# Kernel optimization log

Hardware: AMD Instinct MI355X
Metric: run time of the kernel (lower is better)

## Reference

```python
import jax, jax.numpy as jnp
import numpy as np

N_NODES = 50000
N_EDGES = 1600000
N_GRAPHS = 64
F_IN = 256
H = 1024
EPS = 1e-5


def setup_inputs() -> dict:
    key = jax.random.key(0)
    ks = jax.random.split(key, 6)
    x = jax.random.normal(ks[0], (N_NODES, F_IN), dtype=jnp.float32)
    edge_index = jax.random.randint(ks[1], (2, N_EDGES), 0, N_NODES, dtype=jnp.int32)
    batch = jnp.sort(jax.random.randint(ks[2], (N_NODES,), 0, N_GRAPHS, dtype=jnp.int32))
    # Glorot-ish init for GCN weights
    W0 = jax.random.normal(ks[3], (F_IN, H), dtype=jnp.float32) * (1.0 / np.sqrt(F_IN))
    b0 = jnp.zeros((H,), dtype=jnp.float32)
    Ws = jax.random.normal(ks[4], (3, H, H), dtype=jnp.float32) * (1.0 / np.sqrt(H))
    bs = jnp.zeros((3, H), dtype=jnp.float32)
    gammas = jnp.ones((4, H), dtype=jnp.float32)
    betas = jnp.zeros((4, H), dtype=jnp.float32)
    return {"x": x, "edge_index": edge_index, "batch": batch,
            "W0": W0, "b0": b0, "Ws": Ws, "bs": bs,
            "gammas": gammas, "betas": betas}


def _gcn_norm(edge_index, n_nodes):
    # Add self-loops (PyG GCNConv default), compute symmetric normalization.
    loops = jnp.arange(n_nodes, dtype=edge_index.dtype)
    row = jnp.concatenate([edge_index[0], loops])  # sources
    col = jnp.concatenate([edge_index[1], loops])  # targets (aggregation index)
    ones = jnp.ones(row.shape[0], dtype=jnp.float32)
    deg = jax.ops.segment_sum(ones, col, num_segments=n_nodes)
    dinv = jnp.where(deg > 0, jax.lax.rsqrt(deg), 0.0)
    norm = dinv[row] * dinv[col]  # [E + N]
    return row, col, norm


def _layer(h, W, b, gamma, beta, row, col, norm):
    ht = h @ W                                           # [N, H] GEMM
    msg = ht[row] * norm[:, None]                        # gather + scale
    agg = jax.ops.segment_sum(msg, col, num_segments=N_NODES) + b
    mu = jnp.mean(agg, axis=-1, keepdims=True)
    var = jnp.mean(jnp.square(agg - mu), axis=-1, keepdims=True)
    hn = (agg - mu) * jax.lax.rsqrt(var + EPS) * gamma + beta
    return jax.nn.relu(hn)


def reference(x, edge_index, batch, W0, b0, Ws, bs, gammas, betas):
    row, col, norm = _gcn_norm(edge_index, N_NODES)
    h = _layer(x, W0, b0, gammas[0], betas[0], row, col, norm)
    for i in range(3):
        h = _layer(h, Ws[i], bs[i], gammas[i + 1], betas[i + 1], row, col, norm)
    # scatter_mean over batch (graph-level pooling)
    sums = jax.ops.segment_sum(h, batch, num_segments=N_GRAPHS)
    cnt = jax.ops.segment_sum(jnp.ones((N_NODES,), jnp.float32), batch, num_segments=N_GRAPHS)
    return sums / jnp.maximum(cnt, 1.0)[:, None]
```

## Files before the change

kernel.cpp:

```cpp
#include <hip/hip_runtime.h>
#include <hip/hip_bf16.h>
#include <stdint.h>

#define NN 50000
#define NE 1600000
#define NG 64
#define FIN 256
#define HD 1024
#define EPSV 1e-5f

typedef __bf16 bf16;
typedef float f32x4 __attribute__((ext_vector_type(4)));
typedef float f32x2 __attribute__((ext_vector_type(2)));
typedef int i32x4 __attribute__((ext_vector_type(4)));

typedef const __attribute__((address_space(1))) void* gptr_as1;
typedef __attribute__((address_space(3))) void* lptr_as3;

__device__ __forceinline__ void load_g2l_16(const void* g, const void* l) {
  __builtin_amdgcn_global_load_lds((gptr_as1)(uintptr_t)g,
                                   (lptr_as3)(uint32_t)(uintptr_t)l, 16, 0, 0);
}

__global__ void hist_kernel(const int* __restrict__ col, int* __restrict__ cnt, int E) {
  int e = blockIdx.x * 256 + threadIdx.x;
  if (e < E) atomicAdd(&cnt[col[e]], 1);
}

__global__ void dinv_kernel(const int* __restrict__ cnt, float* __restrict__ dinv, int n) {
  int i = blockIdx.x * 256 + threadIdx.x;
  if (i < n) dinv[i] = rsqrtf((float)(cnt[i] + 1));
}

__global__ void scan_partial_kernel(const int* __restrict__ cnt, int* __restrict__ partial, int n) {
  __shared__ int red[4];
  int i = blockIdx.x * 256 + threadIdx.x;
  int v = (i < n) ? cnt[i] : 0;
  #pragma unroll
  for (int off = 32; off; off >>= 1) v += __shfl_down(v, off, 64);
  if ((threadIdx.x & 63) == 0) red[threadIdx.x >> 6] = v;
  __syncthreads();
  if (threadIdx.x == 0) partial[blockIdx.x] = red[0] + red[1] + red[2] + red[3];
}

__global__ void scan_scan_kernel(int* __restrict__ partial, int nb) {
  __shared__ int s[256];
  int t = threadIdx.x;
  int v = (t < nb) ? partial[t] : 0;
  s[t] = v;
  __syncthreads();
  for (int off = 1; off < 256; off <<= 1) {
    int x = (t >= off) ? s[t - off] : 0;
    __syncthreads();
    s[t] += x;
    __syncthreads();
  }
  if (t < nb) partial[t] = s[t] - v;
}

__global__ void scan_final_kernel(const int* __restrict__ cnt, const int* __restrict__ partial,
                                  int* __restrict__ row_ptr, int n, int E) {
  __shared__ int s[256];
  int t = threadIdx.x;
  int i = blockIdx.x * 256 + t;
  int v = (i < n) ? cnt[i] : 0;
  s[t] = v;
  __syncthreads();
  for (int off = 1; off < 256; off <<= 1) {
    int x = (t >= off) ? s[t - off] : 0;
    __syncthreads();
    s[t] += x;
    __syncthreads();
  }
  if (i < n) row_ptr[i] = partial[blockIdx.x] + s[t] - v;
  if (i == 0) row_ptr[n] = E;
}

__global__ void scatter_kernel(const int* __restrict__ rowi, const int* __restrict__ coli,
                               const int* __restrict__ row_ptr, int* __restrict__ fill,
                               const float* __restrict__ dinv,
                               int2* __restrict__ csr_sw, int E) {
  int e = blockIdx.x * 256 + threadIdx.x;
  if (e >= E) return;
  int s = rowi[e], d = coli[e];
  int pos = row_ptr[d] + atomicAdd(&fill[d], 1);
  int2 p;
  p.x = s;
  p.y = __float_as_int(dinv[s] * dinv[d]);
  csr_sw[pos] = p;
}

__global__ __launch_bounds__(256) void quant_x_kernel(const float* __restrict__ x,
                                                      int8_t* __restrict__ A8,
                                                      float* __restrict__ hscale) {
  int row = blockIdx.x * 4 + (threadIdx.x >> 6);
  int t = threadIdx.x & 63;
  float4 v = ((const float4*)(x + (size_t)row * FIN))[t];
  float m = fmaxf(fmaxf(fabsf(v.x), fabsf(v.y)), fmaxf(fabsf(v.z), fabsf(v.w)));
  #pragma unroll
  for (int off = 32; off; off >>= 1) m = fmaxf(m, __shfl_xor(m, off, 64));
  float inv = (m > 0.f) ? 127.0f / m : 0.f;
  int q0 = min(127, max(-127, __float2int_rn(v.x * inv)));
  int q1 = min(127, max(-127, __float2int_rn(v.y * inv)));
  int q2 = min(127, max(-127, __float2int_rn(v.z * inv)));
  int q3 = min(127, max(-127, __float2int_rn(v.w * inv)));
  uint32_t p = ((uint32_t)(q0 & 0xff)) | ((uint32_t)(q1 & 0xff) << 8) |
               ((uint32_t)(q2 & 0xff) << 16) | ((uint32_t)(q3 & 0xff) << 24);
  ((uint32_t*)A8)[(size_t)row * 64 + t] = p;
  if (t == 0) hscale[row] = (m > 0.f) ? m / 127.0f : 0.f;
}

__device__ __forceinline__ const float* layer_W(const float* W0, const float* Ws, int L) {
  return (L == 0) ? W0 : Ws + (size_t)(L - 1) * HD * HD;
}

__global__ void wamax_all_kernel(const float* __restrict__ W0, const float* __restrict__ Ws,
                                 uint32_t* __restrict__ colmax) {
  __shared__ float lds[8][32];
  int L = blockIdx.z;
  int K = (L == 0) ? FIN : HD;
  int k0 = blockIdx.y * 128;
  if (k0 >= K) return;
  const float* W = layer_W(W0, Ws, L);
  int n = blockIdx.x * 32 + threadIdx.x;
  int kend = min(k0 + 128, K);
  float m = 0.f;
  for (int k = k0 + threadIdx.y; k < kend; k += 8)
    m = fmaxf(m, fabsf(W[(size_t)k * HD + n]));
  lds[threadIdx.y][threadIdx.x] = m;
  __syncthreads();
  if (threadIdx.y == 0) {
    #pragma unroll
    for (int i = 1; i < 8; i++) m = fmaxf(m, lds[i][threadIdx.x]);
    atomicMax(&colmax[L * HD + n], __float_as_uint(m));
  }
}

__global__ void wscale_all_kernel(const uint32_t* __restrict__ colmax,
                                  float* __restrict__ wscale) {
  int i = blockIdx.x * 256 + threadIdx.x;
  if (i < 4 * HD) {
    float m = __uint_as_float(colmax[i]);
    wscale[i] = (m > 0.f) ? m / 127.0f : 0.f;
  }
}

__global__ void transpose_wq8_all_kernel(const float* __restrict__ W0,
                                         const float* __restrict__ Ws,
                                         const uint32_t* __restrict__ colmax,
                                         int8_t* __restrict__ Wt8_all) {
  __shared__ float tile[32][33];
  int L = blockIdx.z;
  int K = (L == 0) ? FIN : HD;
  int k0 = blockIdx.y * 32;
  if (k0 >= K) return;
  const float* W = layer_W(W0, Ws, L);
  int8_t* Wt8 = Wt8_all + ((L == 0) ? 0 : (size_t)FIN * HD + (size_t)(L - 1) * HD * HD);
  int n0 = blockIdx.x * 32;
  int tx = threadIdx.x, ty = threadIdx.y;
  #pragma unroll
  for (int i = ty; i < 32; i += 8) tile[i][tx] = W[(size_t)(k0 + i) * HD + n0 + tx];
  __syncthreads();
  #pragma unroll
  for (int i = ty; i < 32; i += 8) {
    float cm = __uint_as_float(colmax[L * HD + n0 + i]);
    float inv = (cm > 0.f) ? 127.0f / cm : 0.f;
    int q = min(127, max(-127, __float2int_rn(tile[tx][i] * inv)));
    Wt8[(size_t)(n0 + i) * K + k0 + tx] = (int8_t)q;
  }
}

__global__ __launch_bounds__(256, 4) void gemm_i8_q8_kernel(
    const int8_t* __restrict__ A8, const float* __restrict__ hscale,
    const int8_t* __restrict__ Wt8, const float* __restrict__ wscale,
    uint8_t* __restrict__ C8, float* __restrict__ scales, int M, int K) {
  __shared__ __align__(16) int8_t As[2][128 * 64];
  __shared__ __align__(16) int8_t Bs[2][128 * 64];
  __shared__ float smax[2][128];
  const int tid = threadIdx.x;
  const int w = tid >> 6, l = tid & 63;

  const int nwg = gridDim.x;
  const int o = blockIdx.x;
  const int lid = (o & 7) * (nwg >> 3) + (o >> 3);
  const int m0 = (lid >> 3) * 128, n0 = (lid & 7) * 128;
  const int cb = lid & 7;
  const int wr = w >> 1, wc = w & 1;

  i32x4 acc[4][4] = {};

  const int r0 = tid >> 2;
  const int c16 = (tid & 3) * 16;
  int ar0 = m0 + r0;       if (ar0 >= M) ar0 = M - 1;
  int ar1 = m0 + r0 + 64;  if (ar1 >= M) ar1 = M - 1;
  const int8_t* a0 = A8 + (size_t)ar0 * K + c16;
  const int8_t* a1 = A8 + (size_t)ar1 * K + c16;
  const int8_t* b0 = Wt8 + (size_t)(n0 + r0) * K + c16;
  const int8_t* b1 = Wt8 + (size_t)(n0 + r0 + 64) * K + c16;

  const int mrow = l & 15;
  const int kch = (l >> 4) * 16;

  auto stage = [&](int b, int k) {
    int8_t* asw = &As[b][w * 1024];
    int8_t* bsw = &Bs[b][w * 1024];
    load_g2l_16(a0 + k, asw);
    load_g2l_16(a1 + k, asw + 4096);
    load_g2l_16(b0 + k, bsw);
    load_g2l_16(b1 + k, bsw + 4096);
  };

  const int nit = K >> 6;
  stage(0, 0);
  __syncthreads();

  int cur = 0;
  for (int t = 0; t < nit; ++t) {
    if (t + 1 < nit) stage(cur ^ 1, (t + 1) << 6);
    i32x4 af[4], bf_[4];
    #pragma unroll
    for (int m = 0; m < 4; m++)
      af[m] = *(const i32x4*)&As[cur][(wr * 64 + m * 16 + mrow) * 64 + kch];
    #pragma unroll
    for (int n = 0; n < 4; n++)
      bf_[n] = *(const i32x4*)&Bs[cur][(wc * 64 + n * 16 + mrow) * 64 + kch];
    #pragma unroll
    for (int m = 0; m < 4; m++)
      #pragma unroll
      for (int n = 0; n < 4; n++)
        acc[m][n] = __builtin_amdgcn_mfma_i32_16x16x64_i8(af[m], bf_[n], acc[m][n], 0, 0, 0);
    __syncthreads();
    cur ^= 1;
  }

  float wsv[4];
  #pragma unroll
  for (int n = 0; n < 4; n++) wsv[n] = wscale[n0 + wc * 64 + n * 16 + (l & 15)];

  #pragma unroll
  for (int m = 0; m < 4; m++) {
    #pragma unroll
    for (int r = 0; r < 4; r++) {
      int rl = wr * 64 + m * 16 + (l >> 4) * 4 + r;
      int grow = m0 + rl; if (grow >= M) grow = M - 1;
      float v = 0.f;
      #pragma unroll
      for (int n = 0; n < 4; n++)
        v = fmaxf(v, fabsf((float)acc[m][n][r] * wsv[n]));
      v *= hscale[grow];
      #pragma unroll
      for (int mask = 1; mask < 16; mask <<= 1) v = fmaxf(v, __shfl_xor(v, mask, 64));
      if ((l & 15) == 0) smax[wc][rl] = v;
    }
  }
  __syncthreads();

  #pragma unroll
  for (int m = 0; m < 4; m++) {
    #pragma unroll
    for (int r = 0; r < 4; r++) {
      int rl = wr * 64 + m * 16 + (l >> 4) * 4 + r;
      int grow = m0 + rl;
      float mx = fmaxf(smax[0][rl], smax[1][rl]);
      float inv = (mx > 0.f) ? 127.0f / mx : 0.f;
      if (grow < M) {
        float hs = hscale[grow];
        if (wc == 0 && (l & 15) == 0)
          scales[(size_t)grow * 8 + cb] = (mx > 0.f) ? mx / 127.0f : 0.f;
        #pragma unroll
        for (int n = 0; n < 4; n++) {
          int gcol = n0 + wc * 64 + n * 16 + (l & 15);
          int u = __float2int_rn((float)acc[m][n][r] * hs * wsv[n] * inv) + 128;
          C8[(size_t)grow * HD + gcol] = (uint8_t)u;
        }
      }
    }
  }
}

__device__ __forceinline__ void acc_u8p(f32x2 a[4], float& sw, float w, uint2 d) {
  sw += w;
  f32x2 w2 = {w, w};
  f32x2 v0 = {(float)(d.x & 0xffu), (float)((d.x >> 8) & 0xffu)};
  f32x2 v1 = {(float)((d.x >> 16) & 0xffu), (float)(d.x >> 24)};
  f32x2 v2 = {(float)(d.y & 0xffu), (float)((d.y >> 8) & 0xffu)};
  f32x2 v3 = {(float)((d.y >> 16) & 0xffu), (float)(d.y >> 24)};
  a[0] += w2 * v0;
  a[1] += w2 * v1;
  a[2] += w2 * v2;
  a[3] += w2 * v3;
}

__global__ __launch_bounds__(256) void agg_ln_u8_kernel(
    const uint8_t* __restrict__ htu8, const float* __restrict__ scales,
    const int* __restrict__ row_ptr, const int2* __restrict__ csr_sw,
    const float* __restrict__ dinv, const float* __restrict__ bias,
    const float* __restrict__ gamma, const float* __restrict__ beta,
    int8_t* __restrict__ hq, float* __restrict__ hscale) {
  const int g = threadIdx.x >> 7;
  const int node = blockIdx.x * 2 + g;
  const int tt = threadIdx.x & 127;
  const int cbL = tt >> 4;
  const int wid = threadIdx.x >> 6;
  __shared__ float red[4];

  f32x2 acc2[4] = {};
  float sw = 0.f;

  float dn = dinv[node];
  float wself = dn * dn * scales[(size_t)node * 8 + cbL];
  acc_u8p(acc2, sw, wself, ((const uint2*)(htu8 + (size_t)node * HD))[tt]);

  int e = row_ptr[node];
  const int e1 = row_ptr[node + 1];
  for (; e + 4 <= e1; e += 4) {
    int2 p0 = csr_sw[e], p1 = csr_sw[e + 1], p2 = csr_sw[e + 2], p3 = csr_sw[e + 3];
    float w0 = __int_as_float(p0.y) * scales[(size_t)p0.x * 8 + cbL];
    float w1 = __int_as_float(p1.y) * scales[(size_t)p1.x * 8 + cbL];
    float w2 = __int_as_float(p2.y) * scales[(size_t)p2.x * 8 + cbL];
    float w3 = __int_as_float(p3.y) * scales[(size_t)p3.x * 8 + cbL];
    uint2 d0 = ((const uint2*)(htu8 + (size_t)p0.x * HD))[tt];
    uint2 d1 = ((const uint2*)(htu8 + (size_t)p1.x * HD))[tt];
    uint2 d2 = ((const uint2*)(htu8 + (size_t)p2.x * HD))[tt];
    uint2 d3 = ((const uint2*)(htu8 + (size_t)p3.x * HD))[tt];
    acc_u8p(acc2, sw, w0, d0);
    acc_u8p(acc2, sw, w1, d1);
    acc_u8p(acc2, sw, w2, d2);
    acc_u8p(acc2, sw, w3, d3);
  }
  for (; e < e1; e++) {
    int2 p = csr_sw[e];
    float wgt = __int_as_float(p.y) * scales[(size_t)p.x * 8 + cbL];
    acc_u8p(acc2, sw, wgt, ((const uint2*)(htu8 + (size_t)p.x * HD))[tt]);
  }

  float acc[8] = {acc2[0][0], acc2[0][1], acc2[1][0], acc2[1][1],
                  acc2[2][0], acc2[2][1], acc2[3][0], acc2[3][1]};

  const float4* bias2 = (const float4*)bias;
  float4 ba = bias2[tt * 2], bb = bias2[tt * 2 + 1];
  float c128 = 128.0f * sw;
  acc[0] += ba.x - c128; acc[1] += ba.y - c128; acc[2] += ba.z - c128; acc[3] += ba.w - c128;
  acc[4] += bb.x - c128; acc[5] += bb.y - c128; acc[6] += bb.z - c128; acc[7] += bb.w - c128;

  float s = 0.f;
  #pragma unroll
  for (int j = 0; j < 8; j++) s += acc[j];
  #pragma unroll
  for (int off = 32; off; off >>= 1) s += __shfl_down(s, off, 64);
  if ((threadIdx.x & 63) == 0) red[wid] = s;
  __syncthreads();
  float mean = (red[g * 2] + red[g * 2 + 1]) * (1.0f / HD);
  __syncthreads();

  float d[8], s2 = 0.f;
  #pragma unroll
  for (int j = 0; j < 8; j++) { d[j] = acc[j] - mean; s2 += d[j] * d[j]; }
  #pragma unroll
  for (int off = 32; off; off >>= 1) s2 += __shfl_down(s2, off, 64);
  if ((threadIdx.x & 63) == 0) red[wid] = s2;
  __syncthreads();
  float var = (red[g * 2] + red[g * 2 + 1]) * (1.0f / HD);
  float rstd = rsqrtf(var + EPSV);

  const float4* gam2 = (const float4*)gamma;
  const float4* bet2 = (const float4*)beta;
  float4 g0 = gam2[tt * 2], g1 = gam2[tt * 2 + 1];
  float4 be0 = bet2[tt * 2], be1 = bet2[tt * 2 + 1];
  float gv[8] = {g0.x, g0.y, g0.z, g0.w, g1.x, g1.y, g1.z, g1.w};
  float bv[8] = {be0.x, be0.y, be0.z, be0.w, be1.x, be1.y, be1.z, be1.w};
  float o[8];
  float rmax = 0.f;
  #pragma unroll
  for (int j = 0; j < 8; j++) {
    o[j] = fmaxf(d[j] * rstd * gv[j] + bv[j], 0.0f);
    rmax = fmaxf(rmax, o[j]);
  }

  __syncthreads();
  #pragma unroll
  for (int off = 32; off; off >>= 1) rmax = fmaxf(rmax, __shfl_xor(rmax, off, 64));
  if ((threadIdx.x & 63) == 0) red[wid] = rmax;
  __syncthreads();
  float rm = fmaxf(red[g * 2], red[g * 2 + 1]);
  float qinv = (rm > 0.f) ? 127.0f / rm : 0.f;
  int q[8];
  #pragma unroll
  for (int j = 0; j < 8; j++) q[j] = min(127, __float2int_rn(o[j] * qinv));
  uint32_t p0 = ((uint32_t)q[0]) | ((uint32_t)q[1] << 8) | ((uint32_t)q[2] << 16) | ((uint32_t)q[3] << 24);
  uint32_t p1 = ((uint32_t)q[4]) | ((uint32_t)q[5] << 8) | ((uint32_t)q[6] << 16) | ((uint32_t)q[7] << 24);
  uint2 pk; pk.x = p0; pk.y = p1;
  ((uint2*)(hq + (size_t)node * HD))[tt] = pk;
  if (tt == 0) hscale[node] = (rm > 0.f) ? rm / 127.0f : 0.f;
}

__global__ void starts_kernel(const int* __restrict__ batch, int* __restrict__ start,
                              int n, int ngraph) {
  int g = blockIdx.x * blockDim.x + threadIdx.x;
  if (g > ngraph) return;
  int lo = 0, hi = n;
  while (lo < hi) {
    int mid = (lo + hi) >> 1;
    if (batch[mid] < g) lo = mid + 1; else hi = mid;
  }
  start[g] = lo;
}

#define POOL_CHUNKS 8
__global__ void pool_partial_kernel(const int8_t* __restrict__ hq,
                                    const float* __restrict__ hscale,
                                    const int* __restrict__ start,
                                    float* __restrict__ out) {
  int g = blockIdx.y, c = blockIdx.x;
  int t = threadIdx.x;
  int s0 = start[g], s1 = start[g + 1];
  int len = s1 - s0;
  int per = (len + POOL_CHUNKS - 1) / POOL_CHUNKS;
  int a = s0 + c * per;
  int b = min(a + per, s1);
  if (a >= b) return;
  f32x4 acc = {0.f, 0.f, 0.f, 0.f};
  for (int n = a; n < b; n++) {
    float hs = hscale[n];
    uint32_t d = ((const uint32_t*)(hq + (size_t)n * HD))[t];
    acc[0] += hs * (float)(d & 0xffu);
    acc[1] += hs * (float)((d >> 8) & 0xffu);
    acc[2] += hs * (float)((d >> 16) & 0xffu);
    acc[3] += hs * (float)(d >> 24);
  }
  float* o = out + (size_t)g * HD + t * 4;
  atomicAdd(o + 0, acc[0]);
  atomicAdd(o + 1, acc[1]);
  atomicAdd(o + 2, acc[2]);
  atomicAdd(o + 3, acc[3]);
}

__global__ void pool_div_kernel(float* __restrict__ out, const int* __restrict__ start) {
  int i = blockIdx.x * 256 + threadIdx.x;
  if (i >= NG * HD) return;
  int g = i >> 10;
  float c = (float)max(start[g + 1] - start[g], 1);
  out[i] = out[i] / c;
}

extern "C" void kernel_launch(void* const* d_in, const int* in_sizes, int n_in,
                              void* d_out, int out_size, void* d_ws, size_t ws_size,
                              hipStream_t stream) {
  const float* x      = (const float*)d_in[0];
  const int*   eidx   = (const int*)d_in[1];
  const int*   batch  = (const int*)d_in[2];
  const float* W0     = (const float*)d_in[3];
  const float* b0     = (const float*)d_in[4];
  const float* Ws     = (const float*)d_in[5];
  const float* bs     = (const float*)d_in[6];
  const float* gammas = (const float*)d_in[7];
  const float* betas  = (const float*)d_in[8];
  float* out = (float*)d_out;

  const int* erow = eidx;
  const int* ecol = eidx + NE;

  char* ws = (char*)d_ws;
  size_t off = 0;
  auto alloc = [&](size_t bytes) {
    void* p = ws + off;
    off = (off + bytes + 255) & ~(size_t)255;
    return p;
  };
  int*     cnt     = (int*)alloc((size_t)NN * 4);
  int*     row_ptr = (int*)alloc((size_t)(NN + 1) * 4);
  int*     fill    = (int*)alloc((size_t)NN * 4);
  int*     partial = (int*)alloc(256 * 4);
  float*   dinv    = (float*)alloc((size_t)NN * 4);
  int2*    csr_sw  = (int2*)alloc((size_t)NE * 8);
  int8_t*  Wt8     = (int8_t*)alloc((size_t)FIN * HD + 3 * (size_t)HD * HD);
  int8_t*  A8      = (int8_t*)alloc((size_t)NN * HD);
  uint8_t* ht8     = (uint8_t*)alloc((size_t)NN * HD);
  float*   scales  = (float*)alloc((size_t)NN * 8 * 4);
  int*     gstart  = (int*)alloc(65 * 4);

  float*    wscale = (float*)cnt;
  uint32_t* colmax = (uint32_t*)cnt + 4096;
  float*    hscale = (float*)fill;

  hipMemsetAsync(cnt, 0, (size_t)NN * 4, stream);
  hipMemsetAsync(fill, 0, (size_t)NN * 4, stream);
  hipMemsetAsync(out, 0, (size_t)NG * HD * 4, stream);

  hist_kernel<<<(NE + 255) / 256, 256, 0, stream>>>(ecol, cnt, NE);
  dinv_kernel<<<(NN + 255) / 256, 256, 0, stream>>>(cnt, dinv, NN);
  int nb = (NN + 255) / 256;
  scan_partial_kernel<<<nb, 256, 0, stream>>>(cnt, partial, NN);
  scan_scan_kernel<<<1, 256, 0, stream>>>(partial, nb);
  scan_final_kernel<<<nb, 256, 0, stream>>>(cnt, partial, row_ptr, NN, NE);
  scatter_kernel<<<(NE + 255) / 256, 256, 0, stream>>>(erow, ecol, row_ptr, fill, dinv,
                                                       csr_sw, NE);
  starts_kernel<<<1, 128, 0, stream>>>(batch, gstart, NN, NG);

  quant_x_kernel<<<NN / 4, 256, 0, stream>>>(x, A8, hscale);

  hipMemsetAsync(colmax, 0, 4 * HD * 4, stream);
  wamax_all_kernel<<<dim3(HD / 32, 8, 4), dim3(32, 8), 0, stream>>>(W0, Ws, colmax);
  wscale_all_kernel<<<(4 * HD) / 256, 256, 0, stream>>>(colmax, wscale);
  transpose_wq8_all_kernel<<<dim3(HD / 32, HD / 32, 4), dim3(32, 8), 0, stream>>>(
      W0, Ws, colmax, Wt8);

  const int nmt = (NN + 127) / 128;
  for (int L = 0; L < 4; L++) {
    int K = (L == 0) ? FIN : HD;
    const int8_t* WtL = Wt8 + ((L == 0) ? 0 : (size_t)FIN * HD + (size_t)(L - 1) * HD * HD);
    const float* bias = (L == 0) ? b0 : bs + (size_t)(L - 1) * HD;
    gemm_i8_q8_kernel<<<nmt * 8, 256, 0, stream>>>(A8, hscale, WtL, wscale + L * HD,
                                                   ht8, scales, NN, K);
    agg_ln_u8_kernel<<<NN / 2, 256, 0, stream>>>(ht8, scales, row_ptr, csr_sw,
                                                 dinv, bias, gammas + (size_t)L * HD,
                                                 betas + (size_t)L * HD, A8, hscale);
  }

  pool_partial_kernel<<<dim3(POOL_CHUNKS, NG), 256, 0, stream>>>(A8, hscale, gstart, out);
  pool_div_kernel<<<(NG * HD + 255) / 256, 256, 0, stream>>>(out, gstart);
}
```

Measured before the change: 1.544 ms.

## Reorder layer 0 to aggregate 256-wide inputs before the GEMM

For the first layer, aggregation now runs over the 256-wide quantized input features before multiplying by W0, using the identity Â(XW) = (ÂX)W. The separate 1024-wide gather for layer 0 is replaced by a 256-wide gather, followed by the GEMM and a standalone LayerNorm/ReLU/requantize kernel. Inputs are stored as offset uint8, and the aggregated result is requantized to int8 before the GEMM. That adds an extra quantization step, which may change numerical error.

```diff
diff --git a/kernel.cpp b/kernel.cpp
--- a/kernel.cpp
+++ b/kernel.cpp
@@ -91,8 +91,8 @@
 }
 
 __global__ __launch_bounds__(256) void quant_x_kernel(const float* __restrict__ x,
-                                                      int8_t* __restrict__ A8,
-                                                      float* __restrict__ hscale) {
+                                                      uint8_t* __restrict__ X8,
+                                                      float* __restrict__ xscale) {
   int row = blockIdx.x * 4 + (threadIdx.x >> 6);
   int t = threadIdx.x & 63;
   float4 v = ((const float4*)(x + (size_t)row * FIN))[t];
@@ -100,14 +100,167 @@
   #pragma unroll
   for (int off = 32; off; off >>= 1) m = fmaxf(m, __shfl_xor(m, off, 64));
   float inv = (m > 0.f) ? 127.0f / m : 0.f;
-  int q0 = min(127, max(-127, __float2int_rn(v.x * inv)));
-  int q1 = min(127, max(-127, __float2int_rn(v.y * inv)));
-  int q2 = min(127, max(-127, __float2int_rn(v.z * inv)));
-  int q3 = min(127, max(-127, __float2int_rn(v.w * inv)));
+  int q0 = min(127, max(-127, __float2int_rn(v.x * inv))) + 128;
+  int q1 = min(127, max(-127, __float2int_rn(v.y * inv))) + 128;
+  int q2 = min(127, max(-127, __float2int_rn(v.z * inv))) + 128;
+  int q3 = min(127, max(-127, __float2int_rn(v.w * inv))) + 128;
+  uint32_t p = ((uint32_t)q0) | ((uint32_t)q1 << 8) |
+               ((uint32_t)q2 << 16) | ((uint32_t)q3 << 24);
+  ((uint32_t*)X8)[(size_t)row * 64 + t] = p;
+  if (t == 0) xscale[row] = (m > 0.f) ? m / 127.0f : 0.f;
+}
+
+__global__ __launch_bounds__(256) void agg0_kernel(
+    const uint8_t* __restrict__ X8, const float* __restrict__ xscale,
+    const int* __restrict__ row_ptr, const int2* __restrict__ csr_sw,
+    const float* __restrict__ dinv,
+    int8_t* __restrict__ AX8, float* __restrict__ axscale) {
+  const int node = blockIdx.x * 4 + (threadIdx.x >> 6);
+  const int t = threadIdx.x & 63;
+
+  float acc[4] = {};
+  float sw = 0.f;
+
+  float dn = dinv[node];
+  float wself = dn * dn * xscale[node];
+  {
+    uint32_t d = ((const uint32_t*)X8)[(size_t)node * 64 + t];
+    sw += wself;
+    acc[0] += wself * (float)(d & 0xffu);
+    acc[1] += wself * (float)((d >> 8) & 0xffu);
+    acc[2] += wself * (float)((d >> 16) & 0xffu);
+    acc[3] += wself * (float)(d >> 24);
+  }
+
+  int e = row_ptr[node];
+  const int e1 = row_ptr[node + 1];
+  for (; e + 4 <= e1; e += 4) {
+    int2 p0 = csr_sw[e], p1 = csr_sw[e + 1], p2 = csr_sw[e + 2], p3 = csr_sw[e + 3];
+    float w0 = __int_as_float(p0.y) * xscale[p0.x];
+    float w1 = __int_as_float(p1.y) * xscale[p1.x];
+    float w2 = __int_as_float(p2.y) * xscale[p2.x];
+    float w3 = __int_as_float(p3.y) * xscale[p3.x];
+    uint32_t d0 = ((const uint32_t*)X8)[(size_t)p0.x * 64 + t];
+    uint32_t d1 = ((const uint32_t*)X8)[(size_t)p1.x * 64 + t];
+    uint32_t d2 = ((const uint32_t*)X8)[(size_t)p2.x * 64 + t];
+    uint32_t d3 = ((const uint32_t*)X8)[(size_t)p3.x * 64 + t];
+    sw += w0 + w1 + w2 + w3;
+    acc[0] += w0 * (float)(d0 & 0xffu) + w1 * (float)(d1 & 0xffu)
+            + w2 * (float)(d2 & 0xffu) + w3 * (float)(d3 & 0xffu);
+    acc[1] += w0 * (float)((d0 >> 8) & 0xffu) + w1 * (float)((d1 >> 8) & 0xffu)
+            + w2 * (float)((d2 >> 8) & 0xffu) + w3 * (float)((d3 >> 8) & 0xffu);
+    acc[2] += w0 * (float)((d0 >> 16) & 0xffu) + w1 * (float)((d1 >> 16) & 0xffu)
+            + w2 * (float)((d2 >> 16) & 0xffu) + w3 * (float)((d3 >> 16) & 0xffu);
+    acc[3] += w0 * (float)(d0 >> 24) + w1 * (float)(d1 >> 24)
+            + w2 * (float)(d2 >> 24) + w3 * (float)(d3 >> 24);
+  }
+  for (; e < e1; e++) {
+    int2 p = csr_sw[e];
+    float w = __int_as_float(p.y) * xscale[p.x];
+    uint32_t d = ((const uint32_t*)X8)[(size_t)p.x * 64 + t];
+    sw += w;
+    acc[0] += w * (float)(d & 0xffu);
+    acc[1] += w * (float)((d >> 8) & 0xffu);
+    acc[2] += w * (float)((d >> 16) & 0xffu);
+    acc[3] += w * (float)(d >> 24);
+  }
+
+  float c = 128.0f * sw;
+  #pragma unroll
+  for (int j = 0; j < 4; j++) acc[j] -= c;
+
+  float rm = fmaxf(fmaxf(fabsf(acc[0]), fabsf(acc[1])), fmaxf(fabsf(acc[2]), fabsf(acc[3])));
+  #pragma unroll
+  for (int off = 32; off; off >>= 1) rm = fmaxf(rm, __shfl_xor(rm, off, 64));
+  float qinv = (rm > 0.f) ? 127.0f / rm : 0.f;
+  int q0 = min(127, max(-127, __float2int_rn(acc[0] * qinv)));
+  int q1 = min(127, max(-127, __float2int_rn(acc[1] * qinv)));
+  int q2 = min(127, max(-127, __float2int_rn(acc[2] * qinv)));
+  int q3 = min(127, max(-127, __float2int_rn(acc[3] * qinv)));
   uint32_t p = ((uint32_t)(q0 & 0xff)) | ((uint32_t)(q1 & 0xff) << 8) |
                ((uint32_t)(q2 & 0xff) << 16) | ((uint32_t)(q3 & 0xff) << 24);
-  ((uint32_t*)A8)[(size_t)row * 64 + t] = p;
-  if (t == 0) hscale[row] = (m > 0.f) ? m / 127.0f : 0.f;
+  ((uint32_t*)AX8)[(size_t)node * 64 + t] = p;
+  if (t == 0) axscale[node] = (rm > 0.f) ? rm / 127.0f : 0.f;
+}
+
+__global__ __launch_bounds__(256) void ln0_kernel(
+    const uint8_t* __restrict__ htu8, const float* __restrict__ scales,
+    const float* __restrict__ bias, const float* __restrict__ gamma,
+    const float* __restrict__ beta,
+    int8_t* __restrict__ hq, float* __restrict__ hscale) {
+  const int g = threadIdx.x >> 7;
+  const int node = blockIdx.x * 2 + g;
+  const int tt = threadIdx.x & 127;
+  const int cbL = tt >> 4;
+  const int wid = threadIdx.x >> 6;
+  __shared__ float red[4];
+
+  float sc = scales[(size_t)node * 8 + cbL];
+  uint2 dd = ((const uint2*)(htu8 + (size_t)node * HD))[tt];
+  float acc[8];
+  acc[0] = sc * ((float)(dd.x & 0xffu) - 128.f);
+  acc[1] = sc * ((float)((dd.x >> 8) & 0xffu) - 128.f);
+  acc[2] = sc * ((float)((dd.x >> 16) & 0xffu) - 128.f);
+  acc[3] = sc * ((float)(dd.x >> 24) - 128.f);
+  acc[4] = sc * ((float)(dd.y & 0xffu) - 128.f);
+  acc[5] = sc * ((float)((dd.y >> 8) & 0xffu) - 128.f);
+  acc[6] = sc * ((float)((dd.y >> 16) & 0xffu) - 128.f);
+  acc[7] = sc * ((float)(dd.y >> 24) - 128.f);
+
+  const float4* bias2 = (const float4*)bias;
+  float4 ba = bias2[tt * 2], bb = bias2[tt * 2 + 1];
+  acc[0] += ba.x; acc[1] += ba.y; acc[2] += ba.z; acc[3] += ba.w;
+  acc[4] += bb.x; acc[5] += bb.y; acc[6] += bb.z; acc[7] += bb.w;
+
+  float s = 0.f;
+  #pragma unroll
+  for (int j = 0; j < 8; j++) s += acc[j];
+  #pragma unroll
+  for (int off = 32; off; off >>= 1) s += __shfl_down(s, off, 64);
+  if ((threadIdx.x & 63) == 0) red[wid] = s;
+  __syncthreads();
+  float mean = (red[g * 2] + red[g * 2 + 1]) * (1.0f / HD);
+  __syncthreads();
+
+  float d[8], s2 = 0.f;
+  #pragma unroll
+  for (int j = 0; j < 8; j++) { d[j] = acc[j] - mean; s2 += d[j] * d[j]; }
+  #pragma unroll
+  for (int off = 32; off; off >>= 1) s2 += __shfl_down(s2, off, 64);
+  if ((threadIdx.x & 63) == 0) red[wid] = s2;
+  __syncthreads();
+  float var = (red[g * 2] + red[g * 2 + 1]) * (1.0f / HD);
+  float rstd = rsqrtf(var + EPSV);
+
+  const float4* gam2 = (const float4*)gamma;
+  const float4* bet2 = (const float4*)beta;
+  float4 g0 = gam2[tt * 2], g1 = gam2[tt * 2 + 1];
+  float4 be0 = bet2[tt * 2], be1 = bet2[tt * 2 + 1];
+  float gv[8] = {g0.x, g0.y, g0.z, g0.w, g1.x, g1.y, g1.z, g1.w};
+  float bv[8] = {be0.x, be0.y, be0.z, be0.w, be1.x, be1.y, be1.z, be1.w};
+  float o[8];
+  float rmax = 0.f;
+  #pragma unroll
+  for (int j = 0; j < 8; j++) {
+    o[j] = fmaxf(d[j] * rstd * gv[j] + bv[j], 0.0f);
+    rmax = fmaxf(rmax, o[j]);
+  }
+
+  __syncthreads();
+  #pragma unroll
+  for (int off = 32; off; off >>= 1) rmax = fmaxf(rmax, __shfl_xor(rmax, off, 64));
+  if ((threadIdx.x & 63) == 0) red[wid] = rmax;
+  __syncthreads();
+  float rm = fmaxf(red[g * 2], red[g * 2 + 1]);
+  float qinv = (rm > 0.f) ? 127.0f / rm : 0.f;
+  int q[8];
+  #pragma unroll
+  for (int j = 0; j < 8; j++) q[j] = min(127, __float2int_rn(o[j] * qinv));
+  uint32_t p0 = ((uint32_t)q[0]) | ((uint32_t)q[1] << 8) | ((uint32_t)q[2] << 16) | ((uint32_t)q[3] << 24);
+  uint32_t p1 = ((uint32_t)q[4]) | ((uint32_t)q[5] << 8) | ((uint32_t)q[6] << 16) | ((uint32_t)q[7] << 24);
+  uint2 pk; pk.x = p0; pk.y = p1;
+  ((uint2*)(hq + (size_t)node * HD))[tt] = pk;
+  if (tt == 0) hscale[node] = (rm > 0.f) ? rm / 127.0f : 0.f;
 }
 
 __device__ __forceinline__ const float* layer_W(const float* W0, const float* Ws, int L) {
@@ -477,6 +630,10 @@
   int8_t*  A8      = (int8_t*)alloc((size_t)NN * HD);
   uint8_t* ht8     = (uint8_t*)alloc((size_t)NN * HD);
   float*   scales  = (float*)alloc((size_t)NN * 8 * 4);
+  uint8_t* X8      = (uint8_t*)alloc((size_t)NN * FIN);
+  int8_t*  AX8     = (int8_t*)alloc((size_t)NN * FIN);
+  float*   xscale  = (float*)alloc((size_t)NN * 4);
+  float*   axscale = (float*)alloc((size_t)NN * 4);
   int*     gstart  = (int*)alloc(65 * 4);
 
   float*    wscale = (float*)cnt;
@@ -497,7 +654,7 @@
                                                        csr_sw, NE);
   starts_kernel<<<1, 128, 0, stream>>>(batch, gstart, NN, NG);
 
-  quant_x_kernel<<<NN / 4, 256, 0, stream>>>(x, A8, hscale);
+  quant_x_kernel<<<NN / 4, 256, 0, stream>>>(x, X8, xscale);
 
   hipMemsetAsync(colmax, 0, 4 * HD * 4, stream);
   wamax_all_kernel<<<dim3(HD / 32, 8, 4), dim3(32, 8), 0, stream>>>(W0, Ws, colmax);
@@ -506,12 +663,17 @@
       W0, Ws, colmax, Wt8);
 
   const int nmt = (NN + 127) / 128;
-  for (int L = 0; L < 4; L++) {
-    int K = (L == 0) ? FIN : HD;
-    const int8_t* WtL = Wt8 + ((L == 0) ? 0 : (size_t)FIN * HD + (size_t)(L - 1) * HD * HD);
-    const float* bias = (L == 0) ? b0 : bs + (size_t)(L - 1) * HD;
+
+  agg0_kernel<<<NN / 4, 256, 0, stream>>>(X8, xscale, row_ptr, csr_sw, dinv, AX8, axscale);
+  gemm_i8_q8_kernel<<<nmt * 8, 256, 0, stream>>>(AX8, axscale, Wt8, wscale,
+                                                 ht8, scales, NN, FIN);
+  ln0_kernel<<<NN / 2, 256, 0, stream>>>(ht8, scales, b0, gammas, betas, A8, hscale);
+
+  for (int L = 1; L < 4; L++) {
+    const int8_t* WtL = Wt8 + (size_t)FIN * HD + (size_t)(L - 1) * HD * HD;
+    const float* bias = bs + (size_t)(L - 1) * HD;
     gemm_i8_q8_kernel<<<nmt * 8, 256, 0, stream>>>(A8, hscale, WtL, wscale + L * HD,
-                                                   ht8, scales, NN, K);
+                                                   ht8, scales, NN, HD);
     agg_ln_u8_kernel<<<NN / 2, 256, 0, stream>>>(ht8, scales, row_ptr, csr_sw,
                                                  dinv, bias, gammas + (size_t)L * HD,
                                                  betas + (size_t)L * HD, A8, hscale);
```

New measurement: 1.411 ms. 1.09x faster.
